# Kernel optimization log

Measured on AMD Instinct MI355X. Metric: run time of the kernel, lower is better.

The kernel has to match this reference:

```python
import jax, jax.numpy as jnp
import numpy as np

DIM = 2048
H = 16
KV_RANK = 512
NOPE = 128
ROPE_D = 64
VD = 128
QK = NOPE + ROPE_D  # 192
SCALE = QK ** -0.5
B, S = 2, 2048
EPS = 1e-5


def _rope(x, start_pos):
    # x: (b, s, h, d) or (b, s, d); rotate along last dim, positions along axis 1
    s = x.shape[1]
    d = x.shape[-1]
    half = d // 2
    inv_freq = 1.0 / (10000.0 ** (jnp.arange(half, dtype=jnp.float32) * (2.0 / d)))
    pos = jnp.arange(start_pos, start_pos + s, dtype=jnp.float32)
    ang = pos[:, None] * inv_freq[None, :]  # (s, half)
    cos, sin = jnp.cos(ang), jnp.sin(ang)
    if x.ndim == 4:
        cos, sin = cos[None, :, None, :], sin[None, :, None, :]
    else:
        cos, sin = cos[None, :, :], sin[None, :, :]
    x1, x2 = x[..., :half], x[..., half:]
    return jnp.concatenate([x1 * cos - x2 * sin, x2 * cos + x1 * sin], axis=-1).astype(x.dtype)


def _layernorm(x, w, b):
    mu = jnp.mean(x, axis=-1, keepdims=True)
    var = jnp.mean(jnp.square(x - mu), axis=-1, keepdims=True)
    return (x - mu) * jax.lax.rsqrt(var + EPS) * w + b


def setup_inputs() -> dict:
    key = jax.random.key(0)
    ks = jax.random.split(key, 6)
    std = 0.02
    x = jax.random.normal(ks[0], (B, S, DIM), dtype=jnp.float32)
    wq = jax.random.normal(ks[1], (H * QK, DIM), dtype=jnp.float32) * std
    wkv_a = jax.random.normal(ks[2], (KV_RANK + ROPE_D, DIM), dtype=jnp.float32) * std
    wkv_b = jax.random.normal(ks[3], (H * (NOPE + VD), KV_RANK), dtype=jnp.float32) * std
    wo = jax.random.normal(ks[4], (DIM, H * VD), dtype=jnp.float32) * std
    kv_norm_w = jnp.ones((KV_RANK,), dtype=jnp.float32)
    kv_norm_b = jnp.zeros((KV_RANK,), dtype=jnp.float32)
    return {"x": x, "wq": wq, "wkv_a": wkv_a, "kv_norm_w": kv_norm_w,
            "kv_norm_b": kv_norm_b, "wkv_b": wkv_b, "wo": wo, "start_pos": 0}


def reference(x, wq, wkv_a, kv_norm_w, kv_norm_b, wkv_b, wo, start_pos):
    b, s, _ = x.shape
    # query projection: (b,s,H,QK)
    q = (x @ wq.T).reshape(b, s, H, QK)
    q_nope, q_pe = q[..., :NOPE], q[..., NOPE:]
    q_pe = _rope(q_pe, start_pos)
    # compressed kv + rope key
    kv_all = x @ wkv_a.T                      # (b,s,KV_RANK+ROPE_D)
    kv, k_pe = kv_all[..., :KV_RANK], kv_all[..., KV_RANK:]
    k_pe = _rope(k_pe, start_pos)             # (b,s,ROPE_D)
    kvn = _layernorm(kv, kv_norm_w, kv_norm_b)  # (b,s,KV_RANK)
    # absorb path: expand compressed kv through per-head wkv_b blocks
    w = wkv_b.reshape(H, NOPE + VD, KV_RANK)
    k_nope = jnp.einsum('btc,hdc->bthd', kvn, w[:, :NOPE])   # (b,t,H,NOPE)
    v = jnp.einsum('btc,hdc->bthd', kvn, w[:, NOPE:])        # (b,t,H,VD)
    q_full = jnp.concatenate([q_nope, q_pe], axis=-1)        # (b,s,H,QK)
    k_full = jnp.concatenate(
        [k_nope, jnp.broadcast_to(k_pe[:, :, None, :], (b, s, H, ROPE_D))], axis=-1)
    scores = jnp.einsum('bshd,bthd->bhst', q_full, k_full) * SCALE
    causal = jnp.tril(jnp.ones((s, s), dtype=bool))
    scores = jnp.where(causal[None, None], scores, jnp.float32(-1e30))
    attn = jax.nn.softmax(scores, axis=-1)
    out = jnp.einsum('bhst,bthd->bshd', attn, v).reshape(b, s, H * VD)
    return out @ wo.T
```

## Files before the change

kernel.cpp:

```cpp
#include <hip/hip_runtime.h>
#include <hip/hip_bf16.h>
#include <math.h>

typedef __bf16 bf16_t;
typedef __bf16 bf16x2 __attribute__((ext_vector_type(2)));
typedef __bf16 bf16x4 __attribute__((ext_vector_type(4)));
typedef __bf16 bf16x8 __attribute__((ext_vector_type(8)));
typedef float f32x4 __attribute__((ext_vector_type(4)));

#define SEQ 2048
#define MLA_SCALE 0.07216878364870322f
#define LN_EPS 1e-5f

__device__ __forceinline__ void gload_lds16(const bf16_t* g, bf16_t* l) {
    __builtin_amdgcn_global_load_lds(
        (const __attribute__((address_space(1))) uint32_t*)(const void*)g,
        (__attribute__((address_space(3))) uint32_t*)(void*)l, 16, 0, 0);
}

__device__ __forceinline__ void xcd_map(int bid, int total, int nbn,
                                        int& bm, int& bn) {
    int per = total >> 3;
    int cbm = per / nbn;
    int xcd = bid & 7, s = bid >> 3;
    int q = s / nbn;
    bm = xcd * cbm + q;
    bn = s - q * nbn;
}

__global__ __launch_bounds__(256)
void cvt_f32_bf16(const float* __restrict__ in, bf16_t* __restrict__ out, int n4) {
    for (int i = blockIdx.x * 256 + threadIdx.x; i < n4; i += gridDim.x * 256) {
        float4 v = ((const float4*)in)[i];
        bf16x4 p = { (bf16_t)v.x, (bf16_t)v.y, (bf16_t)v.z, (bf16_t)v.w };
        ((bf16x4*)out)[i] = p;
    }
}

#define G256_PHASE(TAU, KS, MH, HTO, MAT, WAITV)                               \
{                                                                              \
    const int slot_ = (2 * (TAU) + (KS)) & 3;                                  \
    bf16x8 af_[4];                                                             \
    {                                                                          \
        const bf16_t* ab_ = As + slot_ * 8192 +                                \
                            (wm2 * 128 + (MH) * 64 + lr) * 32 + rdcol;         \
        _Pragma("unroll")                                                      \
        for (int f = 0; f < 4; ++f) af_[f] = *(const bf16x8*)(ab_ + f * 512);  \
    }                                                                          \
    if ((MH) == 0) {                                                           \
        const bf16_t* bb_ = Bs + slot_ * 8192 + (wn2 * 64 + lr) * 32 + rdcol;  \
        _Pragma("unroll")                                                      \
        for (int f = 0; f < 4; ++f) bq[f] = *(const bf16x8*)(bb_ + f * 512);   \
    }                                                                          \
    if ((MAT) == 0) stageA(2 * T + 3 + (HTO)); else stageB(2 * T + 3 + (HTO)); \
    __builtin_amdgcn_s_barrier();                                              \
    asm volatile("" ::: "memory");                                             \
    __builtin_amdgcn_s_setprio(1);                                             \
    _Pragma("unroll")                                                          \
    for (int f = 0; f < 4; ++f)                                                \
        _Pragma("unroll")                                                      \
        for (int n = 0; n < 4; ++n)                                            \
            acc[(MH) * 4 + f][n] = __builtin_amdgcn_mfma_f32_16x16x32_bf16(    \
                af_[f], bq[n], acc[(MH) * 4 + f][n], 0, 0, 0);                 \
    __builtin_amdgcn_s_setprio(0);                                             \
    asm volatile("" ::: "memory");                                             \
    if (WAITV) asm volatile("s_waitcnt vmcnt(8)" ::: "memory");                \
    __builtin_amdgcn_s_barrier();                                              \
}

template<int MODE>
__global__ __launch_bounds__(512, 2)
void gemm256(const bf16_t* __restrict__ A, const bf16_t* __restrict__ B,
             float* __restrict__ C, bf16_t* __restrict__ out0,
             bf16_t* __restrict__ out1, int N, int K, int total, int nbn) {
    __shared__ __attribute__((aligned(16))) bf16_t As[32768];
    __shared__ __attribute__((aligned(16))) bf16_t Bs[32768];
    __shared__ __attribute__((aligned(16))) bf16_t Ds[8192];

    const int tid = threadIdx.x;
    const int lane = tid & 63, w = tid >> 6;
    const int lr = lane & 15, kh = lane >> 4;
    const int wm2 = w >> 2, wn2 = w & 3;
    int bm, bn;
    xcd_map(blockIdx.x, total, nbn, bm, bn);
    const int NT = K >> 6;

    const int rdcol = 8 * (kh ^ ((lr >> 1) & 3));
    const int strow = (w << 5) + (lane >> 2);
    const int scol = 8 * ((lane & 3) ^ ((lane >> 3) & 3));

    f32x4 acc[8][4];
    #pragma unroll
    for (int i = 0; i < 8; ++i)
        #pragma unroll
        for (int j = 0; j < 4; ++j) acc[i][j] = 0.0f;

    auto stageA = [&](int ht) {
        int hs = (ht < 2 * NT) ? ht : (2 * NT - 1);
        int tau = hs >> 1, kap = hs & 1;
        const bf16_t* g = A + (size_t)(bm * 256 + strow) * K + tau * 64 + kap * 32 + scol;
        bf16_t* l = (ht < 2 * NT) ? (As + (ht & 3) * 8192 + w * 1024) : (Ds + w * 1024);
        gload_lds16(g, l);
        gload_lds16(g + (size_t)16 * K, l + 512);
    };
    auto stageB = [&](int ht) {
        int hs = (ht < 2 * NT) ? ht : (2 * NT - 1);
        int tau = hs >> 1, kap = hs & 1;
        const bf16_t* g = B + (size_t)(bn * 256 + strow) * K + tau * 64 + kap * 32 + scol;
        bf16_t* l = (ht < 2 * NT) ? (Bs + (ht & 3) * 8192 + w * 1024) : (Ds + w * 1024);
        gload_lds16(g, l);
        gload_lds16(g + (size_t)16 * K, l + 512);
    };

    stageA(0); stageB(0); stageA(1); stageB(1); stageA(2); stageB(2);
    asm volatile("s_waitcnt vmcnt(8)" ::: "memory");
    __builtin_amdgcn_s_barrier();

    for (int it = 0; it < (NT >> 1); ++it) {
        const int T = 2 * it;
        bf16x8 bq[4];
        G256_PHASE(T,     0, 0, 0, 0, 0)
        G256_PHASE(T,     0, 1, 0, 1, 1)
        G256_PHASE(T,     1, 0, 1, 0, 0)
        G256_PHASE(T,     1, 1, 1, 1, 1)
        G256_PHASE(T + 1, 0, 0, 2, 0, 0)
        G256_PHASE(T + 1, 0, 1, 2, 1, 1)
        G256_PHASE(T + 1, 1, 0, 3, 0, 0)
        G256_PHASE(T + 1, 1, 1, 3, 1, 1)
    }

    const int rg = kh * 4;
    if (MODE == 0) {
        #pragma unroll
        for (int mf = 0; mf < 8; ++mf)
            #pragma unroll
            for (int nf = 0; nf < 4; ++nf) {
                size_t row0 = (size_t)(bm * 256 + wm2 * 128 + mf * 16 + rg);
                int col = bn * 256 + wn2 * 64 + nf * 16 + lr;
                #pragma unroll
                for (int rr = 0; rr < 4; ++rr)
                    C[(row0 + rr) * N + col] = acc[mf][nf][rr];
            }
    } else if (MODE == 1) {
        const int h = bn;
        #pragma unroll
        for (int mf = 0; mf < 8; ++mf)
            #pragma unroll
            for (int nf = 0; nf < 4; ++nf) {
                int d = wn2 * 64 + nf * 16 + lr;
                int trow = bm * 256 + wm2 * 128 + mf * 16 + rg;
                int b = trow >> 11, t = trow & 2047;
                if (d < 128) {
                    bf16_t* p = out0 + ((size_t)(b * 16 + h) * SEQ + t) * 192 + d;
                    #pragma unroll
                    for (int rr = 0; rr < 4; ++rr)
                        p[rr * 192] = (bf16_t)acc[mf][nf][rr];
                } else {
                    bf16x4 pv = { (bf16_t)acc[mf][nf][0], (bf16_t)acc[mf][nf][1],
                                  (bf16_t)acc[mf][nf][2], (bf16_t)acc[mf][nf][3] };
                    *(bf16x4*)(out1 + ((size_t)(b * 16 + h) * 128 + (d - 128)) * SEQ + t) = pv;
                }
            }
    } else {
        #pragma unroll
        for (int mf = 0; mf < 8; ++mf)
            #pragma unroll
            for (int nf = 0; nf < 4; ++nf) {
                int n = bn * 256 + wn2 * 64 + nf * 16 + lr;
                int h = n / 192, d = n - h * 192;
                int trow = bm * 256 + wm2 * 128 + mf * 16 + rg;
                int b = trow >> 11, t = trow & 2047;
                bf16_t* p = out0 + ((size_t)(b * 16 + h) * SEQ + t) * 192 + d;
                #pragma unroll
                for (int rr = 0; rr < 4; ++rr)
                    p[rr * 192] = (bf16_t)acc[mf][nf][rr];
            }
    }
}

__global__ __launch_bounds__(256)
void gemm_nt(const bf16_t* __restrict__ A, const bf16_t* __restrict__ B,
             float* __restrict__ C, int M, int N, int K, int total, int nbn) {
    __shared__ bf16_t As[4096], Bs[4096];
    int bm, bn;
    xcd_map(blockIdx.x, total, nbn, bm, bn);

    const int tid = threadIdx.x;
    const int lane = tid & 63, w = tid >> 6;
    const int lr = lane & 15, kh = lane >> 4;
    const int wm = (w >> 1) * 64, wn = (w & 1) * 64;
    const int subrow = lane >> 2;
    const int colel = (lane & 3) * 8;

    f32x4 acc[4][4];
    #pragma unroll
    for (int i = 0; i < 4; ++i)
        #pragma unroll
        for (int j = 0; j < 4; ++j) acc[i][j] = 0.0f;

    const int rA = bm * 128 + 32 * w + subrow;
    const int rB = bn * 128 + 32 * w + subrow;
    const int rb1 = (rB < N) ? rB : (N - 1);
    const int rb2 = (rB + 16 < N) ? (rB + 16) : (N - 1);

    for (int kt = 0; kt < K; kt += 32) {
        __syncthreads();
        gload_lds16(A + (size_t)rA * K + kt + colel,        As + (2 * w) * 512);
        gload_lds16(A + (size_t)(rA + 16) * K + kt + colel, As + (2 * w + 1) * 512);
        gload_lds16(B + (size_t)rb1 * K + kt + colel,       Bs + (2 * w) * 512);
        gload_lds16(B + (size_t)rb2 * K + kt + colel,       Bs + (2 * w + 1) * 512);
        __syncthreads();
        bf16x8 af[4], bfr[4];
        #pragma unroll
        for (int im = 0; im < 4; ++im)
            af[im] = *(const bf16x8*)(As + (wm + im * 16 + lr) * 32 + kh * 8);
        #pragma unroll
        for (int jn = 0; jn < 4; ++jn)
            bfr[jn] = *(const bf16x8*)(Bs + (wn + jn * 16 + lr) * 32 + kh * 8);
        #pragma unroll
        for (int im = 0; im < 4; ++im)
            #pragma unroll
            for (int jn = 0; jn < 4; ++jn)
                acc[im][jn] = __builtin_amdgcn_mfma_f32_16x16x32_bf16(
                    af[im], bfr[jn], acc[im][jn], 0, 0, 0);
    }

    const int rg = kh * 4;
    #pragma unroll
    for (int im = 0; im < 4; ++im)
        #pragma unroll
        for (int jn = 0; jn < 4; ++jn) {
            int col = bn * 128 + wn + jn * 16 + lr;
            if (col >= N) continue;
            size_t rowb = (size_t)(bm * 128 + wm + im * 16 + rg);
            #pragma unroll
            for (int rr = 0; rr < 4; ++rr)
                C[(rowb + rr) * N + col] = acc[im][jn][rr];
        }
}

__global__ __launch_bounds__(256)
void rope_ln(const float* __restrict__ kv_all,
             const float* __restrict__ lnw, const float* __restrict__ lnb,
             bf16_t* __restrict__ kvnb, bf16_t* __restrict__ kpack,
             float2* __restrict__ rope_cs, const int* __restrict__ start_pos) {
    const int m = blockIdx.x;
    const int tid = threadIdx.x;
    const int b = m >> 11, t = m & 2047;
    const float pos = (float)(start_pos[0] + t);
    __shared__ float red[8];
    __shared__ float stats[2];
    __shared__ float kbuf[64];

    const float* kvrow = kv_all + (size_t)m * 576;
    float v0 = kvrow[tid], v1 = kvrow[tid + 256];
    float ssum = v0 + v1, ssq = v0 * v0 + v1 * v1;
    for (int off = 32; off > 0; off >>= 1) {
        ssum += __shfl_down(ssum, off);
        ssq  += __shfl_down(ssq, off);
    }
    const int lane = tid & 63, wid = tid >> 6;
    if (lane == 0) { red[wid] = ssum; red[4 + wid] = ssq; }
    __syncthreads();
    if (tid == 0) {
        float ts = red[0] + red[1] + red[2] + red[3];
        float tq = red[4] + red[5] + red[6] + red[7];
        float mu = ts * (1.0f / 512.0f);
        float var = tq * (1.0f / 512.0f) - mu * mu;
        stats[0] = mu;
        stats[1] = rsqrtf(var + LN_EPS);
    }
    if (tid < 32) {
        int j = tid;
        float inv = expf(-(float)j * 0.2878231366242554f);
        float ang = pos * inv;
        float c = cosf(ang), sn = sinf(ang);
        float x1 = kvrow[512 + j], x2 = kvrow[544 + j];
        kbuf[j]      = x1 * c - x2 * sn;
        kbuf[32 + j] = x2 * c + x1 * sn;
        if (b == 0) rope_cs[t * 32 + j] = make_float2(c, sn);
    }
    __syncthreads();
    float mu = stats[0], rstd = stats[1];
    kvnb[(size_t)m * 512 + tid]       = (bf16_t)((v0 - mu) * rstd * lnw[tid] + lnb[tid]);
    kvnb[(size_t)m * 512 + tid + 256] = (bf16_t)((v1 - mu) * rstd * lnw[tid + 256] + lnb[tid + 256]);

    {
        int hh = tid >> 4, j4 = (tid & 15) * 4;
        bf16x4 pk = { (bf16_t)kbuf[j4], (bf16_t)kbuf[j4 + 1],
                      (bf16_t)kbuf[j4 + 2], (bf16_t)kbuf[j4 + 3] };
        *(bf16x4*)(kpack + ((size_t)(b * 16 + hh) * SEQ + t) * 192 + 128 + j4) = pk;
    }
}

__global__ __launch_bounds__(256, 2)
void attn_mfma(const bf16_t* __restrict__ qb, const bf16_t* __restrict__ kpack,
               const bf16_t* __restrict__ vt, const float2* __restrict__ rope_cs,
               bf16_t* __restrict__ ao) {
    __shared__ bf16_t Ks[64][200];
    __shared__ bf16_t Vts[128][72];
    __shared__ bf16_t Pls[4][16][72];

    const int bid = blockIdx.x;
    const int xcd = bid & 7, s = bid >> 3;
    const int g = xcd * 4 + (s >> 4);
    const int bx = s & 15;
    const int h = g & 15, b = g >> 4;

    const int tid = threadIdx.x;
    const int lane = tid & 63, w = tid >> 6;
    const int lr = lane & 15, kh = lane >> 4;
    const size_t bS = (size_t)b * SEQ;
    const bf16_t* kbase = kpack + (size_t)(b * 16 + h) * SEQ * 192;
    const bf16_t* vbase = vt + (size_t)(b * 16 + h) * 128 * SEQ;

    int krow_[6], koff_[6], vd_[4], vt8_[4];
    #pragma unroll
    for (int i = 0; i < 6; ++i) { int c = tid + 256 * i; krow_[i] = c / 24; koff_[i] = (c % 24) * 8; }
    #pragma unroll
    for (int i = 0; i < 4; ++i) { int c = tid + 256 * i; vd_[i] = c >> 3; vt8_[i] = (c & 7) * 8; }

    for (int half = 0; half < 2; ++half) {
        const int qt = half ? bx : (31 - bx);
        const int q0 = qt * 64;
        const int myrow = q0 + w * 16;
        const int qabs = myrow + lr;

        bf16x8 qf[6];
        {
            const bf16_t* qrow = qb + ((size_t)(b * 16 + h) * SEQ + qabs) * 192;
            #pragma unroll
            for (int ks = 0; ks < 6; ++ks)
                qf[ks] = *(const bf16x8*)(qrow + ks * 32 + kh * 8);
            const float2* csp = rope_cs + (size_t)qabs * 32 + kh * 8;
            #pragma unroll
            for (int i = 0; i < 8; ++i) {
                float2 cs = csp[i];
                float x1 = (float)qf[4][i], x2 = (float)qf[5][i];
                qf[4][i] = (bf16_t)(x1 * cs.x - x2 * cs.y);
                qf[5][i] = (bf16_t)(x2 * cs.x + x1 * cs.y);
            }
        }

        f32x4 O[8];
        #pragma unroll
        for (int i = 0; i < 8; ++i) O[i] = 0.0f;
        float m_r = -1e30f, l_r = 0.0f;

        bf16x8 rk[6], rv[4];
        #pragma unroll
        for (int i = 0; i < 6; ++i)
            rk[i] = *(const bf16x8*)(kbase + (size_t)krow_[i] * 192 + koff_[i]);
        #pragma unroll
        for (int i = 0; i < 4; ++i)
            rv[i] = *(const bf16x8*)(vbase + (size_t)vd_[i] * SEQ + vt8_[i]);

        for (int kt = 0; kt <= qt; ++kt) {
            __syncthreads();
            #pragma unroll
            for (int i = 0; i < 6; ++i) *(bf16x8*)&Ks[krow_[i]][koff_[i]] = rk[i];
            #pragma unroll
            for (int i = 0; i < 4; ++i) *(bf16x8*)&Vts[vd_[i]][vt8_[i]] = rv[i];
            if (kt < qt) {
                const int t1 = (kt + 1) * 64;
                #pragma unroll
                for (int i = 0; i < 6; ++i)
                    rk[i] = *(const bf16x8*)(kbase + (size_t)(t1 + krow_[i]) * 192 + koff_[i]);
                #pragma unroll
                for (int i = 0; i < 4; ++i)
                    rv[i] = *(const bf16x8*)(vbase + (size_t)vd_[i] * SEQ + t1 + vt8_[i]);
            }
            __syncthreads();

            f32x4 sacc[4];
            #pragma unroll
            for (int j = 0; j < 4; ++j) sacc[j] = 0.0f;
            __builtin_amdgcn_s_setprio(1);
            #pragma unroll
            for (int ks = 0; ks < 6; ++ks)
                #pragma unroll
                for (int j = 0; j < 4; ++j) {
                    bf16x8 kf = *(const bf16x8*)&Ks[j * 16 + lr][ks * 32 + kh * 8];
                    sacc[j] = __builtin_amdgcn_mfma_f32_16x16x32_bf16(kf, qf[ks], sacc[j], 0, 0, 0);
                }
            __builtin_amdgcn_s_setprio(0);

            const int t0 = kt * 64;
            float p[16];
            if (kt == qt) {
                #pragma unroll
                for (int j = 0; j < 4; ++j)
                    #pragma unroll
                    for (int rr = 0; rr < 4; ++rr) {
                        int tabs = t0 + j * 16 + kh * 4 + rr;
                        p[j * 4 + rr] = (tabs > qabs) ? -1e30f : sacc[j][rr] * MLA_SCALE;
                    }
            } else {
                #pragma unroll
                for (int j = 0; j < 4; ++j)
                    #pragma unroll
                    for (int rr = 0; rr < 4; ++rr)
                        p[j * 4 + rr] = sacc[j][rr] * MLA_SCALE;
            }

            float mx = p[0];
            #pragma unroll
            for (int e = 1; e < 16; ++e) mx = fmaxf(mx, p[e]);
            mx = fmaxf(mx, __shfl_xor(mx, 16));
            mx = fmaxf(mx, __shfl_xor(mx, 32));

            if (!__all(mx <= m_r + 8.0f)) {
                float mnew = fmaxf(m_r, mx);
                float cr = __expf(m_r - mnew);
                l_r *= cr;
                m_r = mnew;
                float corr[4];
                #pragma unroll
                for (int rr = 0; rr < 4; ++rr)
                    corr[rr] = __shfl(cr, kh * 4 + rr);
                #pragma unroll
                for (int dt = 0; dt < 8; ++dt)
                    #pragma unroll
                    for (int rr = 0; rr < 4; ++rr)
                        O[dt][rr] *= corr[rr];
            }

            float ps = 0.0f;
            #pragma unroll
            for (int e = 0; e < 16; ++e) {
                p[e] = __expf(p[e] - m_r);
                ps += p[e];
            }
            ps += __shfl_xor(ps, 16);
            ps += __shfl_xor(ps, 32);
            l_r += ps;

            #pragma unroll
            for (int j = 0; j < 4; ++j) {
                bf16x4 pp = { (bf16_t)p[j * 4], (bf16_t)p[j * 4 + 1],
                              (bf16_t)p[j * 4 + 2], (bf16_t)p[j * 4 + 3] };
                *(bf16x4*)&Pls[w][lr][j * 16 + kh * 4] = pp;
            }
            bf16x8 pa0 = *(const bf16x8*)&Pls[w][lr][kh * 8];
            bf16x8 pa1 = *(const bf16x8*)&Pls[w][lr][32 + kh * 8];
            __builtin_amdgcn_s_setprio(1);
            #pragma unroll
            for (int dt = 0; dt < 8; ++dt) {
                bf16x8 b0 = *(const bf16x8*)&Vts[dt * 16 + lr][kh * 8];
                O[dt] = __builtin_amdgcn_mfma_f32_16x16x32_bf16(pa0, b0, O[dt], 0, 0, 0);
                bf16x8 b1 = *(const bf16x8*)&Vts[dt * 16 + lr][32 + kh * 8];
                O[dt] = __builtin_amdgcn_mfma_f32_16x16x32_bf16(pa1, b1, O[dt], 0, 0, 0);
            }
            __builtin_amdgcn_s_setprio(0);
        }

        float linv[4];
        #pragma unroll
        for (int rr = 0; rr < 4; ++rr)
            linv[rr] = 1.0f / __shfl(l_r, kh * 4 + rr);
        #pragma unroll
        for (int rr = 0; rr < 4; ++rr) {
            size_t rowb = (bS + myrow + kh * 4 + rr) * 2048 + h * 128;
            #pragma unroll
            for (int dt = 0; dt < 8; ++dt)
                ao[rowb + dt * 16 + lr] = (bf16_t)(O[dt][rr] * linv[rr]);
        }
    }
}

extern "C" void kernel_launch(void* const* d_in, const int* in_sizes, int n_in,
                              void* d_out, int out_size, void* d_ws, size_t ws_size,
                              hipStream_t stream) {
    const float* x     = (const float*)d_in[0];
    const float* wq    = (const float*)d_in[1];
    const float* wkv_a = (const float*)d_in[2];
    const float* lnw   = (const float*)d_in[3];
    const float* lnb   = (const float*)d_in[4];
    const float* wkv_b = (const float*)d_in[5];
    const float* wo    = (const float*)d_in[6];
    const int* start_pos = (const int*)d_in[7];
    float* out = (float*)d_out;

    char* w8 = (char*)d_ws;
    bf16_t* xb   = (bf16_t*)(w8);
    bf16_t* wqb  = (bf16_t*)(w8 + 16777216);
    bf16_t* wab  = (bf16_t*)(w8 + 29360128);
    bf16_t* wbb  = (bf16_t*)(w8 + 31719424);
    bf16_t* wob  = (bf16_t*)(w8 + 35913728);
    bf16_t* kvnb = (bf16_t*)(w8 + 44302336);
    bf16_t* kpk  = (bf16_t*)(w8 + 48496640);
    bf16_t* vtb  = (bf16_t*)(w8 + 73662464);
    bf16_t* aob  = (bf16_t*)(w8 + 90439680);
    bf16_t* qbh  = (bf16_t*)(w8 + 107216896);
    float*  kva  = (float*)(w8 + 132382720);
    float2* rcs  = (float2*)(w8 + 141819904);

    cvt_f32_bf16<<<2048, 256, 0, stream>>>(x,     xb,  8388608 / 4);
    cvt_f32_bf16<<<2048, 256, 0, stream>>>(wq,    wqb, 6291456 / 4);
    cvt_f32_bf16<<<1152, 256, 0, stream>>>(wkv_a, wab, 1179648 / 4);
    cvt_f32_bf16<<<2048, 256, 0, stream>>>(wkv_b, wbb, 2097152 / 4);
    cvt_f32_bf16<<<2048, 256, 0, stream>>>(wo,    wob, 4194304 / 4);

    gemm256<2><<<192, 512, 0, stream>>>(xb, wqb, nullptr, qbh, nullptr, 3072, 2048, 192, 12);
    gemm_nt<<<160, 256, 0, stream>>>(xb, wab, kva, 4096, 576, 2048, 160, 5);
    rope_ln<<<4096, 256, 0, stream>>>(kva, lnw, lnb, kvnb, kpk, rcs, start_pos);
    gemm256<1><<<256, 512, 0, stream>>>(kvnb, wbb, nullptr, kpk, vtb, 4096, 512, 256, 16);
    attn_mfma<<<512, 256, 0, stream>>>(qbh, kpk, vtb, rcs, aob);
    gemm_nt<<<512, 256, 0, stream>>>(aob, wob, out, 4096, 2048, 2048, 512, 16);
}
```

Before: 287.6 us.

## Swizzle attention LDS layouts, split query tiles per block, fuse conversions

```diff
diff --git a/kernel.cpp b/kernel.cpp
--- a/kernel.cpp
+++ b/kernel.cpp
@@ -28,12 +28,29 @@
     bn = s - q * nbn;
 }
 
+#define CVT_N0 2097152
+#define CVT_N1 1572864
+#define CVT_N2 294912
+#define CVT_N3 524288
+#define CVT_N4 1048576
+#define CVT_TOT (CVT_N0 + CVT_N1 + CVT_N2 + CVT_N3 + CVT_N4)
+
 __global__ __launch_bounds__(256)
-void cvt_f32_bf16(const float* __restrict__ in, bf16_t* __restrict__ out, int n4) {
-    for (int i = blockIdx.x * 256 + threadIdx.x; i < n4; i += gridDim.x * 256) {
-        float4 v = ((const float4*)in)[i];
+void cvt_all(const float* __restrict__ x, const float* __restrict__ wq,
+             const float* __restrict__ wa, const float* __restrict__ wb,
+             const float* __restrict__ wo, bf16_t* __restrict__ xb,
+             bf16_t* __restrict__ wqb, bf16_t* __restrict__ wab,
+             bf16_t* __restrict__ wbb, bf16_t* __restrict__ wob) {
+    for (int i = blockIdx.x * 256 + threadIdx.x; i < CVT_TOT; i += gridDim.x * 256) {
+        const float* src; bf16_t* dst; int off = i;
+        if (i < CVT_N0) { src = x; dst = xb; }
+        else if (i < CVT_N0 + CVT_N1) { src = wq; dst = wqb; off = i - CVT_N0; }
+        else if (i < CVT_N0 + CVT_N1 + CVT_N2) { src = wa; dst = wab; off = i - CVT_N0 - CVT_N1; }
+        else if (i < CVT_N0 + CVT_N1 + CVT_N2 + CVT_N3) { src = wb; dst = wbb; off = i - CVT_N0 - CVT_N1 - CVT_N2; }
+        else { src = wo; dst = wob; off = i - CVT_N0 - CVT_N1 - CVT_N2 - CVT_N3; }
+        float4 v = ((const float4*)src)[off];
         bf16x4 p = { (bf16_t)v.x, (bf16_t)v.y, (bf16_t)v.z, (bf16_t)v.w };
-        ((bf16x4*)out)[i] = p;
+        ((bf16x4*)dst)[off] = p;
     }
 }
 
@@ -293,178 +310,195 @@
     }
 }
 
-__global__ __launch_bounds__(256, 2)
+__global__ __launch_bounds__(256, 3)
 void attn_mfma(const bf16_t* __restrict__ qb, const bf16_t* __restrict__ kpack,
                const bf16_t* __restrict__ vt, const float2* __restrict__ rope_cs,
                bf16_t* __restrict__ ao) {
-    __shared__ bf16_t Ks[64][200];
-    __shared__ bf16_t Vts[128][72];
-    __shared__ bf16_t Pls[4][16][72];
+    __shared__ bf16_t Ks[64 * 192];
+    __shared__ bf16_t Vts[128 * 64];
+    __shared__ bf16_t Pls[4 * 16 * 64];
 
     const int bid = blockIdx.x;
     const int xcd = bid & 7, s = bid >> 3;
-    const int g = xcd * 4 + (s >> 4);
-    const int bx = s & 15;
+    const int g = xcd * 4 + (s >> 5);
+    const int qt = 31 - (s & 31);
     const int h = g & 15, b = g >> 4;
 
     const int tid = threadIdx.x;
     const int lane = tid & 63, w = tid >> 6;
     const int lr = lane & 15, kh = lane >> 4;
+    const int lr7 = lr & 7;
+    const int e0 = kh ^ lr7;
+    const int e1 = (4 + kh) ^ lr7;
     const size_t bS = (size_t)b * SEQ;
     const bf16_t* kbase = kpack + (size_t)(b * 16 + h) * SEQ * 192;
     const bf16_t* vbase = vt + (size_t)(b * 16 + h) * 128 * SEQ;
 
-    int krow_[6], koff_[6], vd_[4], vt8_[4];
-    #pragma unroll
-    for (int i = 0; i < 6; ++i) { int c = tid + 256 * i; krow_[i] = c / 24; koff_[i] = (c % 24) * 8; }
-    #pragma unroll
-    for (int i = 0; i < 4; ++i) { int c = tid + 256 * i; vd_[i] = c >> 3; vt8_[i] = (c & 7) * 8; }
-
-    for (int half = 0; half < 2; ++half) {
-        const int qt = half ? bx : (31 - bx);
-        const int q0 = qt * 64;
-        const int myrow = q0 + w * 16;
-        const int qabs = myrow + lr;
-
-        bf16x8 qf[6];
-        {
-            const bf16_t* qrow = qb + ((size_t)(b * 16 + h) * SEQ + qabs) * 192;
-            #pragma unroll
-            for (int ks = 0; ks < 6; ++ks)
-                qf[ks] = *(const bf16x8*)(qrow + ks * 32 + kh * 8);
-            const float2* csp = rope_cs + (size_t)qabs * 32 + kh * 8;
-            #pragma unroll
-            for (int i = 0; i < 8; ++i) {
-                float2 cs = csp[i];
-                float x1 = (float)qf[4][i], x2 = (float)qf[5][i];
-                qf[4][i] = (bf16_t)(x1 * cs.x - x2 * cs.y);
-                qf[5][i] = (bf16_t)(x2 * cs.x + x1 * cs.y);
+    int kgo_[6], klo_[6], vgo_[4], vlo_[4];
+    #pragma unroll
+    for (int i = 0; i < 6; ++i) {
+        int c = tid + 256 * i;
+        int row = c / 24, slot = c % 24;
+        kgo_[i] = row * 192 + slot * 8;
+        klo_[i] = row * 192 + ((slot & 24) | ((slot ^ row) & 7)) * 8;
+    }
+    #pragma unroll
+    for (int i = 0; i < 4; ++i) {
+        int c = tid + 256 * i;
+        int row = c >> 3, slot = c & 7;
+        vgo_[i] = row;
+        vlo_[i] = row * 64 + (slot ^ (row & 7)) * 8;
+    }
+    int vco_[4];
+    #pragma unroll
+    for (int i = 0; i < 4; ++i) vco_[i] = (tid + 256 * i) & 7;
+
+    const int q0 = qt * 64;
+    const int myrow = q0 + w * 16;
+    const int qabs = myrow + lr;
+
+    bf16x8 qf[6];
+    {
+        const bf16_t* qrow = qb + ((size_t)(b * 16 + h) * SEQ + qabs) * 192;
+        #pragma unroll
+        for (int ks = 0; ks < 6; ++ks)
+            qf[ks] = *(const bf16x8*)(qrow + ks * 32 + kh * 8);
+        const float2* csp = rope_cs + (size_t)qabs * 32 + kh * 8;
+        #pragma unroll
+        for (int i = 0; i < 8; ++i) {
+            float2 cs = csp[i];
+            float x1 = (float)qf[4][i], x2 = (float)qf[5][i];
+            qf[4][i] = (bf16_t)(x1 * cs.x - x2 * cs.y);
+            qf[5][i] = (bf16_t)(x2 * cs.x + x1 * cs.y);
+        }
+    }
+
+    f32x4 O[8];
+    #pragma unroll
+    for (int i = 0; i < 8; ++i) O[i] = 0.0f;
+    float m_r = -1e30f, l_r = 0.0f;
+
+    bf16x8 rk[6], rv[4];
+    #pragma unroll
+    for (int i = 0; i < 6; ++i)
+        rk[i] = *(const bf16x8*)(kbase + kgo_[i]);
+    #pragma unroll
+    for (int i = 0; i < 4; ++i)
+        rv[i] = *(const bf16x8*)(vbase + (size_t)vgo_[i] * SEQ + vco_[i] * 8);
+
+    for (int kt = 0; kt <= qt; ++kt) {
+        __syncthreads();
+        #pragma unroll
+        for (int i = 0; i < 6; ++i) *(bf16x8*)(Ks + klo_[i]) = rk[i];
+        #pragma unroll
+        for (int i = 0; i < 4; ++i) *(bf16x8*)(Vts + vlo_[i]) = rv[i];
+        if (kt < qt) {
+            const int t1 = (kt + 1) * 64;
+            #pragma unroll
+            for (int i = 0; i < 6; ++i)
+                rk[i] = *(const bf16x8*)(kbase + (size_t)t1 * 192 + kgo_[i]);
+            #pragma unroll
+            for (int i = 0; i < 4; ++i)
+                rv[i] = *(const bf16x8*)(vbase + (size_t)vgo_[i] * SEQ + t1 + vco_[i] * 8);
+        }
+        __syncthreads();
+
+        f32x4 sacc[4];
+        #pragma unroll
+        for (int j = 0; j < 4; ++j) sacc[j] = 0.0f;
+        __builtin_amdgcn_s_setprio(1);
+        #pragma unroll
+        for (int ks = 0; ks < 6; ++ks) {
+            const int sw = (ks >> 1) * 64 + ((ks & 1) ? e1 : e0) * 8;
+            #pragma unroll
+            for (int j = 0; j < 4; ++j) {
+                bf16x8 kf = *(const bf16x8*)(Ks + (j * 16 + lr) * 192 + sw);
+                sacc[j] = __builtin_amdgcn_mfma_f32_16x16x32_bf16(kf, qf[ks], sacc[j], 0, 0, 0);
             }
         }
-
-        f32x4 O[8];
-        #pragma unroll
-        for (int i = 0; i < 8; ++i) O[i] = 0.0f;
-        float m_r = -1e30f, l_r = 0.0f;
-
-        bf16x8 rk[6], rv[4];
-        #pragma unroll
-        for (int i = 0; i < 6; ++i)
-            rk[i] = *(const bf16x8*)(kbase + (size_t)krow_[i] * 192 + koff_[i]);
-        #pragma unroll
-        for (int i = 0; i < 4; ++i)
-            rv[i] = *(const bf16x8*)(vbase + (size_t)vd_[i] * SEQ + vt8_[i]);
-
-        for (int kt = 0; kt <= qt; ++kt) {
-            __syncthreads();
-            #pragma unroll
-            for (int i = 0; i < 6; ++i) *(bf16x8*)&Ks[krow_[i]][koff_[i]] = rk[i];
-            #pragma unroll
-            for (int i = 0; i < 4; ++i) *(bf16x8*)&Vts[vd_[i]][vt8_[i]] = rv[i];
-            if (kt < qt) {
-                const int t1 = (kt + 1) * 64;
+        __builtin_amdgcn_s_setprio(0);
+
+        const int t0 = kt * 64;
+        float p[16];
+        if (kt == qt) {
+            #pragma unroll
+            for (int j = 0; j < 4; ++j)
                 #pragma unroll
-                for (int i = 0; i < 6; ++i)
-                    rk[i] = *(const bf16x8*)(kbase + (size_t)(t1 + krow_[i]) * 192 + koff_[i]);
-                #pragma unroll
-                for (int i = 0; i < 4; ++i)
-                    rv[i] = *(const bf16x8*)(vbase + (size_t)vd_[i] * SEQ + t1 + vt8_[i]);
-            }
-            __syncthreads();
-
-            f32x4 sacc[4];
-            #pragma unroll
-            for (int j = 0; j < 4; ++j) sacc[j] = 0.0f;
-            __builtin_amdgcn_s_setprio(1);
-            #pragma unroll
-            for (int ks = 0; ks < 6; ++ks)
-                #pragma unroll
-                for (int j = 0; j < 4; ++j) {
-                    bf16x8 kf = *(const bf16x8*)&Ks[j * 16 + lr][ks * 32 + kh * 8];
-                    sacc[j] = __builtin_amdgcn_mfma_f32_16x16x32_bf16(kf, qf[ks], sacc[j], 0, 0, 0);
+                for (int rr = 0; rr < 4; ++rr) {
+                    int tabs = t0 + j * 16 + kh * 4 + rr;
+                    p[j * 4 + rr] = (tabs > qabs) ? -1e30f : sacc[j][rr] * MLA_SCALE;
                 }
-            __builtin_amdgcn_s_setprio(0);
-
-            const int t0 = kt * 64;
-            float p[16];
-            if (kt == qt) {
-                #pragma unroll
-                for (int j = 0; j < 4; ++j)
-                    #pragma unroll
-                    for (int rr = 0; rr < 4; ++rr) {
-                        int tabs = t0 + j * 16 + kh * 4 + rr;
-                        p[j * 4 + rr] = (tabs > qabs) ? -1e30f : sacc[j][rr] * MLA_SCALE;
-                    }
-            } else {
-                #pragma unroll
-                for (int j = 0; j < 4; ++j)
-                    #pragma unroll
-                    for (int rr = 0; rr < 4; ++rr)
-                        p[j * 4 + rr] = sacc[j][rr] * MLA_SCALE;
-            }
-
-            float mx = p[0];
-            #pragma unroll
-            for (int e = 1; e < 16; ++e) mx = fmaxf(mx, p[e]);
-            mx = fmaxf(mx, __shfl_xor(mx, 16));
-            mx = fmaxf(mx, __shfl_xor(mx, 32));
-
-            if (!__all(mx <= m_r + 8.0f)) {
-                float mnew = fmaxf(m_r, mx);
-                float cr = __expf(m_r - mnew);
-                l_r *= cr;
-                m_r = mnew;
-                float corr[4];
+        } else {
+            #pragma unroll
+            for (int j = 0; j < 4; ++j)
                 #pragma unroll
                 for (int rr = 0; rr < 4; ++rr)
-                    corr[rr] = __shfl(cr, kh * 4 + rr);
+                    p[j * 4 + rr] = sacc[j][rr] * MLA_SCALE;
+        }
+
+        float mx = p[0];
+        #pragma unroll
+        for (int e = 1; e < 16; ++e) mx = fmaxf(mx, p[e]);
+        mx = fmaxf(mx, __shfl_xor(mx, 16));
+        mx = fmaxf(mx, __shfl_xor(mx, 32));
+
+        if (!__all(mx <= m_r + 8.0f)) {
+            float mnew = fmaxf(m_r, mx);
+            float cr = __expf(m_r - mnew);
+            l_r *= cr;
+            m_r = mnew;
+            float corr[4];
+            #pragma unroll
+            for (int rr = 0; rr < 4; ++rr)
+                corr[rr] = __shfl(cr, kh * 4 + rr);
+            #pragma unroll
+            for (int dt = 0; dt < 8; ++dt)
                 #pragma unroll
-                for (int dt = 0; dt < 8; ++dt)
-                    #pragma unroll
-                    for (int rr = 0; rr < 4; ++rr)
-                        O[dt][rr] *= corr[rr];
-            }
-
-            float ps = 0.0f;
-            #pragma unroll
-            for (int e = 0; e < 16; ++e) {
-                p[e] = __expf(p[e] - m_r);
-                ps += p[e];
-            }
-            ps += __shfl_xor(ps, 16);
-            ps += __shfl_xor(ps, 32);
-            l_r += ps;
-
-            #pragma unroll
-            for (int j = 0; j < 4; ++j) {
-                bf16x4 pp = { (bf16_t)p[j * 4], (bf16_t)p[j * 4 + 1],
-                              (bf16_t)p[j * 4 + 2], (bf16_t)p[j * 4 + 3] };
-                *(bf16x4*)&Pls[w][lr][j * 16 + kh * 4] = pp;
-            }
-            bf16x8 pa0 = *(const bf16x8*)&Pls[w][lr][kh * 8];
-            bf16x8 pa1 = *(const bf16x8*)&Pls[w][lr][32 + kh * 8];
-            __builtin_amdgcn_s_setprio(1);
-            #pragma unroll
-            for (int dt = 0; dt < 8; ++dt) {
-                bf16x8 b0 = *(const bf16x8*)&Vts[dt * 16 + lr][kh * 8];
-                O[dt] = __builtin_amdgcn_mfma_f32_16x16x32_bf16(pa0, b0, O[dt], 0, 0, 0);
-                bf16x8 b1 = *(const bf16x8*)&Vts[dt * 16 + lr][32 + kh * 8];
-                O[dt] = __builtin_amdgcn_mfma_f32_16x16x32_bf16(pa1, b1, O[dt], 0, 0, 0);
-            }
-            __builtin_amdgcn_s_setprio(0);
-        }
-
-        float linv[4];
-        #pragma unroll
-        for (int rr = 0; rr < 4; ++rr)
-            linv[rr] = 1.0f / __shfl(l_r, kh * 4 + rr);
-        #pragma unroll
-        for (int rr = 0; rr < 4; ++rr) {
-            size_t rowb = (bS + myrow + kh * 4 + rr) * 2048 + h * 128;
-            #pragma unroll
-            for (int dt = 0; dt < 8; ++dt)
-                ao[rowb + dt * 16 + lr] = (bf16_t)(O[dt][rr] * linv[rr]);
-        }
+                for (int rr = 0; rr < 4; ++rr)
+                    O[dt][rr] *= corr[rr];
+        }
+
+        float ps = 0.0f;
+        #pragma unroll
+        for (int e = 0; e < 16; ++e) {
+            p[e] = __expf(p[e] - m_r);
+            ps += p[e];
+        }
+        ps += __shfl_xor(ps, 16);
+        ps += __shfl_xor(ps, 32);
+        l_r += ps;
+
+        bf16_t* pw = Pls + (w * 16 + lr) * 64;
+        const int f2 = kh >> 1, h4 = (kh & 1) * 4;
+        #pragma unroll
+        for (int j = 0; j < 4; ++j) {
+            bf16x4 pp = { (bf16_t)p[j * 4], (bf16_t)p[j * 4 + 1],
+                          (bf16_t)p[j * 4 + 2], (bf16_t)p[j * 4 + 3] };
+            *(bf16x4*)(pw + ((2 * j + f2) ^ lr7) * 8 + h4) = pp;
+        }
+        bf16x8 pa0 = *(const bf16x8*)(pw + e0 * 8);
+        bf16x8 pa1 = *(const bf16x8*)(pw + e1 * 8);
+        __builtin_amdgcn_s_setprio(1);
+        #pragma unroll
+        for (int dt = 0; dt < 8; ++dt) {
+            bf16x8 b0 = *(const bf16x8*)(Vts + (dt * 16 + lr) * 64 + e0 * 8);
+            O[dt] = __builtin_amdgcn_mfma_f32_16x16x32_bf16(pa0, b0, O[dt], 0, 0, 0);
+            bf16x8 b1 = *(const bf16x8*)(Vts + (dt * 16 + lr) * 64 + e1 * 8);
+            O[dt] = __builtin_amdgcn_mfma_f32_16x16x32_bf16(pa1, b1, O[dt], 0, 0, 0);
+        }
+        __builtin_amdgcn_s_setprio(0);
+    }
+
+    float linv[4];
+    #pragma unroll
+    for (int rr = 0; rr < 4; ++rr)
+        linv[rr] = 1.0f / __shfl(l_r, kh * 4 + rr);
+    #pragma unroll
+    for (int rr = 0; rr < 4; ++rr) {
+        size_t rowb = (bS + myrow + kh * 4 + rr) * 2048 + h * 128;
+        #pragma unroll
+        for (int dt = 0; dt < 8; ++dt)
+            ao[rowb + dt * 16 + lr] = (bf16_t)(O[dt][rr] * linv[rr]);
     }
 }
 
@@ -495,16 +529,12 @@
     float*  kva  = (float*)(w8 + 132382720);
     float2* rcs  = (float2*)(w8 + 141819904);
 
-    cvt_f32_bf16<<<2048, 256, 0, stream>>>(x,     xb,  8388608 / 4);
-    cvt_f32_bf16<<<2048, 256, 0, stream>>>(wq,    wqb, 6291456 / 4);
-    cvt_f32_bf16<<<1152, 256, 0, stream>>>(wkv_a, wab, 1179648 / 4);
-    cvt_f32_bf16<<<2048, 256, 0, stream>>>(wkv_b, wbb, 2097152 / 4);
-    cvt_f32_bf16<<<2048, 256, 0, stream>>>(wo,    wob, 4194304 / 4);
+    cvt_all<<<2048, 256, 0, stream>>>(x, wq, wkv_a, wkv_b, wo, xb, wqb, wab, wbb, wob);
 
     gemm256<2><<<192, 512, 0, stream>>>(xb, wqb, nullptr, qbh, nullptr, 3072, 2048, 192, 12);
     gemm_nt<<<160, 256, 0, stream>>>(xb, wab, kva, 4096, 576, 2048, 160, 5);
     rope_ln<<<4096, 256, 0, stream>>>(kva, lnw, lnb, kvnb, kpk, rcs, start_pos);
     gemm256<1><<<256, 512, 0, stream>>>(kvnb, wbb, nullptr, kpk, vtb, 4096, 512, 256, 16);
-    attn_mfma<<<512, 256, 0, stream>>>(qbh, kpk, vtb, rcs, aob);
+    attn_mfma<<<1024, 256, 0, stream>>>(qbh, kpk, vtb, rcs, aob);
     gemm_nt<<<512, 256, 0, stream>>>(aob, wob, out, 4096, 2048, 2048, 512, 16);
 }
```

After: 301.2 us. 1.05x slower.
